# Optimization experiments

Hardware: AMD Instinct MI355X
Metric: run time of the kernel (lower is better)

## Reference

```python
import jax, jax.numpy as jnp
import numpy as np

N = 100000   # points
C = 256      # in_planes
K = 16       # nsample (idx holds 2*K neighbors)
L = 2        # num_mlplayer
NEG = 0.1    # LeakyReLU slope
EPS = 1e-5   # LayerNorm eps (torch default)

PARAM_KEYS = ['emb_w1','emb_g1','emb_b1','emb_w2','conv_w','pw_w1','pw_g1','pw_b1','pw_w2','pw_g2','pw_b2']


def layer_norm(x, g, b):
    m = x.mean(-1, keepdims=True)
    v = ((x - m) ** 2).mean(-1, keepdims=True)
    return (x - m) * jax.lax.rsqrt(v + EPS) * g + b


def calc_ppf(p, n, pg, ng):
    # standard 4-dim point-pair features: angle(n1,d), angle(n2,d), angle(n1,n2), ||d||
    d = pg - p[:, None, :]                                   # [N,2K,3]
    dist = jnp.linalg.norm(d, axis=-1, keepdims=True)
    def angle(a, b):
        cr = jnp.linalg.norm(jnp.cross(a, b), axis=-1, keepdims=True)
        dt = jnp.sum(a * b, axis=-1, keepdims=True)
        return jnp.arctan2(cr, dt)
    n1 = jnp.broadcast_to(n[:, None, :], pg.shape)
    return jnp.concatenate([angle(n1, d), angle(ng, d), angle(n1, ng), dist], -1)


def mlp_layer(p, x, idx, ppf, r, pr):
    # cart2sphere -> r-normalized radial distance, giving 4+1=5 embedding inputs
    d = p[idx] - p[:, None, :]                               # [N,K,3]
    sphere = jnp.linalg.norm(d, axis=-1, keepdims=True) / r  # [N,K,1]
    f5 = jnp.concatenate([ppf, sphere], -1)                  # [N,K,5]
    h = f5 @ pr['emb_w1']
    h = jax.nn.leaky_relu(layer_norm(h, pr['emb_g1'], pr['emb_b1']), NEG)
    pos = h @ pr['emb_w2']                                   # [N,K,C]
    g = x[idx] + pos                                         # gather + add
    # Partial_conv3 (split_cat): 1x1 conv (no bias) on first C//4 channels
    c4 = pr['conv_w'].shape[0]
    g1 = jnp.einsum('nkc,dc->nkd', g[..., :c4], pr['conv_w'])
    g = jnp.concatenate([g1, g[..., c4:]], -1)
    pooled = g.max(axis=1)                                   # max-pool over neighbors [N,C]
    h = pooled @ pr['pw_w1']
    h = jax.nn.leaky_relu(layer_norm(h, pr['pw_g1'], pr['pw_b1']), NEG)
    h = layer_norm(h @ pr['pw_w2'], pr['pw_g2'], pr['pw_b2'])
    return jax.nn.relu(h + x)                                # residual + relu


def setup_inputs():
    key = jax.random.key(0)
    ks = jax.random.split(key, 16)
    s = 0.02
    n = jax.random.normal(ks[2], (N, 3), jnp.float32)
    n = n / jnp.linalg.norm(n, axis=-1, keepdims=True)
    return {
        'p': jax.random.normal(ks[0], (N, 3), jnp.float32),
        'x': jax.random.normal(ks[1], (N, C), jnp.float32),
        'n': n,
        'idx': jax.random.randint(ks[3], (N, 2 * K), 0, N, jnp.int32),
        'r': jnp.ones((1,), jnp.float32),
        'emb_w1': jax.random.normal(ks[4], (L, 5, C), jnp.float32) * s,
        'emb_g1': jnp.ones((L, C), jnp.float32),
        'emb_b1': jnp.zeros((L, C), jnp.float32),
        'emb_w2': jax.random.normal(ks[5], (L, C, C), jnp.float32) * s,
        'conv_w': jax.random.normal(ks[6], (L, C // 4, C // 4), jnp.float32) * s,
        'pw_w1': jax.random.normal(ks[7], (L, C, 4 * C), jnp.float32) * s,
        'pw_g1': jnp.ones((L, 4 * C), jnp.float32),
        'pw_b1': jnp.zeros((L, 4 * C), jnp.float32),
        'pw_w2': jax.random.normal(ks[8], (L, 4 * C, C), jnp.float32) * s,
        'pw_g2': jnp.ones((L, C), jnp.float32),
        'pw_b2': jnp.zeros((L, C), jnp.float32),
        'proj_w': jax.random.normal(ks[9], (C, C), jnp.float32) * s,
        'proj_b': jnp.zeros((C,), jnp.float32),
    }


def reference(p, x, n, idx, r, emb_w1, emb_g1, emb_b1, emb_w2, conv_w,
              pw_w1, pw_g1, pw_b1, pw_w2, pw_g2, pw_b2, proj_w, proj_b):
    # idx is given -> group_idx = idx (queryandgroup branch skipped, as in source)
    ppf = calc_ppf(p, n, p[idx], n[idx])                     # [N,2K,4]
    idx_m, ppf_m = idx[:, :K], ppf[:, :K]                    # mlp branch uses first nsample
    stacked = [emb_w1, emb_g1, emb_b1, emb_w2, conv_w, pw_w1, pw_g1, pw_b1, pw_w2, pw_g2, pw_b2]
    h = x
    for l in range(L):
        pr = dict(zip(PARAM_KEYS, [a[l] for a in stacked]))
        h = mlp_layer(p, h, idx_m, ppf_m, r[0], pr)
    # proj_mlp; blocks=1 -> trans_block is an empty Sequential (identity)
    return h @ proj_w + proj_b
```

## Files before the change

kernel.cpp:

```cpp
#include <hip/hip_runtime.h>
#include <stdint.h>

#define N_PTS 100000
#define NPAD  100032

typedef unsigned short u16;
typedef unsigned int   u32;
using bf16x8 = __attribute__((ext_vector_type(8))) short;
using f32x4  = __attribute__((ext_vector_type(4))) float;

__device__ __forceinline__ u16 f2bf(float f) {
    u32 u = __float_as_uint(f);
    u += 0x7FFFu + ((u >> 16) & 1u);
    return (u16)(u >> 16);
}
__device__ __forceinline__ float bf2f(u16 h) {
    return __uint_as_float(((u32)h) << 16);
}

__global__ __launch_bounds__(256) void k_transpose_pad(
    const float* __restrict__ src, u16* __restrict__ dst,
    int Lc, int R, int Cc, int stride) {
    int t = blockIdx.x * 256 + threadIdx.x;
    int total = Lc * Cc * stride;
    if (t >= total) return;
    int l = t / (Cc * stride);
    int rem = t - l * (Cc * stride);
    int co = rem / stride;
    int ci = rem - co * stride;
    dst[t] = (ci < R) ? f2bf(src[((size_t)l * R + ci) * Cc + co]) : (u16)0;
}

__global__ __launch_bounds__(256) void k_cast_bf16(
    const float* __restrict__ src, u16* __restrict__ dst, int total) {
    int t = blockIdx.x * 256 + threadIdx.x;
    if (t < total) dst[t] = f2bf(src[t]);
}

__global__ __launch_bounds__(256) void k_castx8(
    const float* __restrict__ src, u16* __restrict__ dst, int total8) {
    int t = blockIdx.x * 256 + threadIdx.x;
    if (t >= total8) return;
    float4 a = *(const float4*)(src + (size_t)t * 8);
    float4 b = *(const float4*)(src + (size_t)t * 8 + 4);
    uint4 o;
    o.x = (u32)f2bf(a.x) | ((u32)f2bf(a.y) << 16);
    o.y = (u32)f2bf(a.z) | ((u32)f2bf(a.w) << 16);
    o.z = (u32)f2bf(b.x) | ((u32)f2bf(b.y) << 16);
    o.w = (u32)f2bf(b.z) | ((u32)f2bf(b.w) << 16);
    *(uint4*)(dst + (size_t)t * 8) = o;
}

__device__ __forceinline__ float angf(float ax, float ay, float az,
                                      float bx, float by, float bz) {
    float cx = ay * bz - az * by;
    float cy = az * bx - ax * bz;
    float cz = ax * by - ay * bx;
    float cr = sqrtf(cx * cx + cy * cy + cz * cz);
    float dt = ax * bx + ay * by + az * bz;
    return atan2f(cr, dt);
}

__global__ __launch_bounds__(256) void k_ppf(
    const float* __restrict__ p, const float* __restrict__ nrm,
    const int* __restrict__ idx, const float* __restrict__ r,
    u16* __restrict__ f5b) {
    int t = blockIdx.x * 256 + threadIdx.x;
    if (t >= N_PTS * 16) return;
    int i = t >> 4;
    int j = idx[(size_t)i * 32 + (t & 15)];
    float pix = p[(size_t)i*3], piy = p[(size_t)i*3+1], piz = p[(size_t)i*3+2];
    float pjx = p[(size_t)j*3], pjy = p[(size_t)j*3+1], pjz = p[(size_t)j*3+2];
    float dx = pjx - pix, dy = pjy - piy, dz = pjz - piz;
    float dist = sqrtf(dx*dx + dy*dy + dz*dz);
    float nix = nrm[(size_t)i*3], niy = nrm[(size_t)i*3+1], niz = nrm[(size_t)i*3+2];
    float njx = nrm[(size_t)j*3], njy = nrm[(size_t)j*3+1], njz = nrm[(size_t)j*3+2];
    float a1 = angf(nix, niy, niz, dx, dy, dz);
    float a2 = angf(njx, njy, njz, dx, dy, dz);
    float a3 = angf(nix, niy, niz, njx, njy, njz);
    float rinv = 1.0f / r[0];
    u16* o = f5b + (size_t)t * 5;
    o[0] = f2bf(a1); o[1] = f2bf(a2); o[2] = f2bf(a3);
    o[3] = f2bf(dist); o[4] = f2bf(dist * rinv);
}

__device__ __forceinline__ bf16x8 fixup_frag(const uint2* pk, int kt,
                                             int srcA, int srcB, bool hiT) {
    int aLx = __shfl((int)pk[2*kt].x,   srcA);
    int aHx = __shfl((int)pk[2*kt+1].x, srcA);
    int aLy = __shfl((int)pk[2*kt].y,   srcA);
    int aHy = __shfl((int)pk[2*kt+1].y, srcA);
    int bLx = __shfl((int)pk[2*kt].x,   srcB);
    int bHx = __shfl((int)pk[2*kt+1].x, srcB);
    int bLy = __shfl((int)pk[2*kt].y,   srcB);
    int bHy = __shfl((int)pk[2*kt+1].y, srcB);
    uint4 u;
    u.x = (u32)(hiT ? aHx : aLx);
    u.y = (u32)(hiT ? aHy : aLy);
    u.z = (u32)(hiT ? bHx : bLx);
    u.w = (u32)(hiT ? bHy : bLy);
    return *(bf16x8*)&u;
}

__global__ __launch_bounds__(512, 4) void k_neighbor(
    const u16*   __restrict__ xcur,
    const u16*   __restrict__ f5b,
    const int*   __restrict__ idx,
    const u16*   __restrict__ w1pad,
    const float* __restrict__ g1, const float* __restrict__ b1,
    const u16*   __restrict__ ew2tp,
    const u16*   __restrict__ convbf,
    u16*         __restrict__ pooledb)
{
    __shared__ u16 Bs[64 * 264];
    __shared__ u16 posw[8][2][16][72];
    __shared__ u16 pbounce[8][2][256];
    __shared__ int idxs[16][16];

    const int tid = threadIdx.x, w = tid >> 6, lane = tid & 63;
    const int rr = lane & 15, q = lane >> 4;
    const int i0 = blockIdx.x * 16;

    for (int o = tid * 16; o < 33792; o += 8192)
        *(uint4*)((char*)Bs + o) = *(const uint4*)((const char*)ew2tp + o);
    if (tid < 256)
        idxs[tid >> 4][tid & 15] = idx[(size_t)(i0 + (tid >> 4)) * 32 + (tid & 15)];

    const int srcA = rr + ((q & 1) << 5);
    const int srcB = srcA + 16;
    const bool hiT = (q >> 1) != 0;

    bf16x8 hfrag[2][8];
    #pragma unroll
    for (int rt = 0; rt < 2; ++rt) {
        const int pt = i0 + 2 * w + rt;
        bf16x8 a1;
        #pragma unroll
        for (int e = 0; e < 8; ++e) a1[e] = 0;
        if (q == 0) {
            const u16* fp = f5b + (size_t)(pt * 16 + rr) * 5;
            a1[0] = (short)fp[0]; a1[1] = (short)fp[1];
            a1[2] = (short)fp[2]; a1[3] = (short)fp[3];
            a1[4] = (short)fp[4];
        }
        f32x4 hacc[16];
        #pragma unroll
        for (int ct = 0; ct < 16; ++ct) {
            bf16x8 aW = *(const bf16x8*)&w1pad[(ct * 16 + rr) * 32 + q * 8];
            f32x4 z = {0.f, 0.f, 0.f, 0.f};
            hacc[ct] = __builtin_amdgcn_mfma_f32_16x16x32_bf16(aW, a1, z, 0, 0, 0);
        }
        float s = 0.f, z2 = 0.f;
        #pragma unroll
        for (int ct = 0; ct < 16; ++ct) {
            #pragma unroll
            for (int j = 0; j < 4; ++j) { float v = hacc[ct][j]; s += v; z2 += v * v; }
        }
        s  += __shfl_xor(s, 16);  s  += __shfl_xor(s, 32);
        z2 += __shfl_xor(z2, 16); z2 += __shfl_xor(z2, 32);
        float mean = s * (1.f / 256.f);
        float var = fmaxf(z2 * (1.f / 256.f) - mean * mean, 0.f);
        float rstd = 1.0f / sqrtf(var + 1e-5f);

        uint2 pk[16];
        #pragma unroll
        for (int ct = 0; ct < 16; ++ct) {
            const int c0 = ct * 16 + 4 * q;
            float4 gg = *(const float4*)&g1[c0];
            float4 bb = *(const float4*)&b1[c0];
            float v0 = (hacc[ct][0] - mean) * rstd * gg.x + bb.x;
            float v1 = (hacc[ct][1] - mean) * rstd * gg.y + bb.y;
            float v2 = (hacc[ct][2] - mean) * rstd * gg.z + bb.z;
            float v3 = (hacc[ct][3] - mean) * rstd * gg.w + bb.w;
            v0 = v0 > 0.f ? v0 : 0.1f * v0;
            v1 = v1 > 0.f ? v1 : 0.1f * v1;
            v2 = v2 > 0.f ? v2 : 0.1f * v2;
            v3 = v3 > 0.f ? v3 : 0.1f * v3;
            pk[ct].x = (u32)f2bf(v0) | ((u32)f2bf(v1) << 16);
            pk[ct].y = (u32)f2bf(v2) | ((u32)f2bf(v3) << 16);
        }
        #pragma unroll
        for (int kt = 0; kt < 8; ++kt)
            hfrag[rt][kt] = fixup_frag(pk, kt, srcA, srcB, hiT);
    }
    __syncthreads();

    const int ppt = lane >> 5, cl = lane & 31;
    const int* ixp = idxs[2 * w + ppt];

    #pragma unroll 1
    for (int p = 0; p < 4; ++p) {
        #pragma unroll
        for (int nt4 = 0; nt4 < 4; ++nt4) {
            f32x4 a0 = {0.f,0.f,0.f,0.f}, a1v = {0.f,0.f,0.f,0.f};
            #pragma unroll
            for (int kb = 0; kb < 8; ++kb) {
                bf16x8 bb = *(const bf16x8*)&Bs[(nt4 * 16 + rr) * 264 + kb * 32 + q * 8];
                a0  = __builtin_amdgcn_mfma_f32_16x16x32_bf16(hfrag[0][kb], bb, a0, 0, 0, 0);
                a1v = __builtin_amdgcn_mfma_f32_16x16x32_bf16(hfrag[1][kb], bb, a1v, 0, 0, 0);
            }
            #pragma unroll
            for (int j = 0; j < 4; ++j) {
                posw[w][0][4 * q + j][nt4 * 16 + rr] = f2bf(a0[j]);
                posw[w][1][4 * q + j][nt4 * 16 + rr] = f2bf(a1v[j]);
            }
        }
        if (p < 3) {
            __syncthreads();
            const char* src = (const char*)(ew2tp + (size_t)(p + 1) * 64 * 264);
            for (int o = tid * 16; o < 33792; o += 8192)
                *(uint4*)((char*)Bs + o) = *(const uint4*)(src + o);
        }
        if (p == 0) {
            #pragma unroll
            for (int pt = 0; pt < 2; ++pt) {
                const u16* xr = xcur + (size_t)idxs[2 * w + pt][rr] * 256;
                bf16x8 gA[2];
                #pragma unroll
                for (int kb = 0; kb < 2; ++kb) {
                    bf16x8 xa = *(const bf16x8*)(xr + kb * 32 + q * 8);
                    bf16x8 pv = *(const bf16x8*)&posw[w][pt][rr][kb * 32 + q * 8];
                    bf16x8 g;
                    #pragma unroll
                    for (int e = 0; e < 8; ++e)
                        g[e] = (short)f2bf(bf2f((u16)xa[e]) + bf2f((u16)pv[e]));
                    gA[kb] = g;
                }
                #pragma unroll
                for (int cn = 0; cn < 4; ++cn) {
                    bf16x8 cB0 = *(const bf16x8*)&convbf[(cn * 16 + rr) * 64 + q * 8];
                    bf16x8 cB1 = *(const bf16x8*)&convbf[(cn * 16 + rr) * 64 + 32 + q * 8];
                    f32x4 z = {0.f,0.f,0.f,0.f};
                    f32x4 acc = __builtin_amdgcn_mfma_f32_16x16x32_bf16(gA[0], cB0, z, 0, 0, 0);
                    acc = __builtin_amdgcn_mfma_f32_16x16x32_bf16(gA[1], cB1, acc, 0, 0, 0);
                    float m = fmaxf(fmaxf(acc[0], acc[1]), fmaxf(acc[2], acc[3]));
                    m = fmaxf(m, __shfl_xor(m, 16));
                    m = fmaxf(m, __shfl_xor(m, 32));
                    if (lane < 16) pbounce[w][pt][cn * 16 + lane] = f2bf(m);
                }
            }
        } else {
            const int cq = p * 64 + cl * 2;
            u32 xv[16];
            #pragma unroll
            for (int k = 0; k < 16; ++k)
                xv[k] = *(const u32*)(xcur + (size_t)ixp[k] * 256 + cq);
            float m0 = -3e38f, m1 = -3e38f;
            #pragma unroll
            for (int k = 0; k < 16; ++k) {
                u32 pv = *(const u32*)&posw[w][ppt][k][cl * 2];
                float gv0 = bf2f((u16)(pv & 0xffffu)) + bf2f((u16)(xv[k] & 0xffffu));
                float gv1 = bf2f((u16)(pv >> 16))     + bf2f((u16)(xv[k] >> 16));
                m0 = fmaxf(m0, gv0);
                m1 = fmaxf(m1, gv1);
            }
            *(u32*)&pbounce[w][ppt][cq] = (u32)f2bf(m0) | ((u32)f2bf(m1) << 16);
        }
        if (p < 3) __syncthreads();
    }
    {
        const int pt = lane >> 5, off = (lane & 31) * 8;
        uint4 v = *(const uint4*)&pbounce[w][pt][off];
        *(uint4*)(pooledb + (size_t)(i0 + 2 * w + pt) * 256 + off) = v;
    }
}

__global__ __launch_bounds__(512, 4) void k_pointwise(
    const u16* poolb,
    const u16* __restrict__ xresb,
    u16*       outb,
    const u16* __restrict__ b1t,
    const float* __restrict__ g1, const float* __restrict__ b1,
    const u16* __restrict__ b2t,
    const float* __restrict__ g2, const float* __restrict__ b2,
    int guardRes)
{
    __shared__ u16 hm[32 * 1032];
    __shared__ float pst[32][8][2];

    const int tid = threadIdx.x, w = tid >> 6, lane = tid & 63;
    const int rr = lane & 15, q = lane >> 4;
    const size_t R0 = (size_t)blockIdx.x * 32;

    bf16x8 afr[2][8];
    #pragma unroll
    for (int rt = 0; rt < 2; ++rt) {
        int ar = (int)R0 + rt * 16 + rr; if (ar >= N_PTS) ar = N_PTS - 1;
        const u16* arow = poolb + (size_t)ar * 256;
        #pragma unroll
        for (int kb = 0; kb < 8; ++kb)
            afr[rt][kb] = *(const bf16x8*)(arow + kb * 32 + q * 8);
    }

    #pragma unroll 2
    for (int ct = 0; ct < 8; ++ct) {
        const int co = w * 128 + ct * 16 + rr;
        const u16* bp = b1t + (size_t)co * 256 + q * 8;
        bf16x8 bb[8];
        #pragma unroll
        for (int kb = 0; kb < 8; ++kb) bb[kb] = *(const bf16x8*)(bp + kb * 32);
        f32x4 a0 = {0.f,0.f,0.f,0.f}, a1v = {0.f,0.f,0.f,0.f};
        #pragma unroll
        for (int kb = 0; kb < 8; ++kb) {
            a0  = __builtin_amdgcn_mfma_f32_16x16x32_bf16(afr[0][kb], bb[kb], a0, 0, 0, 0);
            a1v = __builtin_amdgcn_mfma_f32_16x16x32_bf16(afr[1][kb], bb[kb], a1v, 0, 0, 0);
        }
        #pragma unroll
        for (int j = 0; j < 4; ++j) {
            hm[(4 * q + j) * 1032 + co]      = f2bf(a0[j]);
            hm[(16 + 4 * q + j) * 1032 + co] = f2bf(a1v[j]);
        }
    }
    __syncthreads();

    {
        const int row = tid >> 4;
        const int t16 = tid & 15;
        u32* hm32 = (u32*)hm;
        const int base = row * 516;
        float s = 0.f, z = 0.f;
        #pragma unroll 8
        for (int e = 0; e < 32; ++e) {
            u32 pk = hm32[base + t16 + 16 * e];
            float v0 = bf2f((u16)(pk & 0xffffu)), v1 = bf2f((u16)(pk >> 16));
            s += v0 + v1; z += v0 * v0 + v1 * v1;
        }
        s += __shfl_xor(s, 1); s += __shfl_xor(s, 2);
        s += __shfl_xor(s, 4); s += __shfl_xor(s, 8);
        z += __shfl_xor(z, 1); z += __shfl_xor(z, 2);
        z += __shfl_xor(z, 4); z += __shfl_xor(z, 8);
        float mean = s * (1.f / 1024.f);
        float var = fmaxf(z * (1.f / 1024.f) - mean * mean, 0.f);
        float rstd = 1.0f / sqrtf(var + 1e-5f);
        #pragma unroll 4
        for (int e = 0; e < 32; ++e) {
            const int cidx = t16 + 16 * e;
            u32 pk = hm32[base + cidx];
            const int c = cidx * 2;
            float2 gg = *(const float2*)&g1[c];
            float2 bbv = *(const float2*)&b1[c];
            float v0 = (bf2f((u16)(pk & 0xffffu)) - mean) * rstd * gg.x + bbv.x;
            float v1 = (bf2f((u16)(pk >> 16))     - mean) * rstd * gg.y + bbv.y;
            v0 = v0 > 0.f ? v0 : 0.1f * v0;
            v1 = v1 > 0.f ? v1 : 0.1f * v1;
            hm32[base + cidx] = (u32)f2bf(v0) | ((u32)f2bf(v1) << 16);
        }
    }
    __syncthreads();

    f32x4 acc2[2][2];
    #pragma unroll
    for (int ct = 0; ct < 2; ++ct) {
        const int cB = w * 32 + ct * 16 + rr;
        const u16* bp = b2t + (size_t)cB * 1024 + q * 8;
        f32x4 c0 = {0.f,0.f,0.f,0.f}, c1 = {0.f,0.f,0.f,0.f};
        #pragma unroll 8
        for (int kb = 0; kb < 32; ++kb) {
            bf16x8 b  = *(const bf16x8*)(bp + kb * 32);
            bf16x8 a0 = *(const bf16x8*)&hm[rr * 1032 + kb * 32 + q * 8];
            bf16x8 a1 = *(const bf16x8*)&hm[(16 + rr) * 1032 + kb * 32 + q * 8];
            c0 = __builtin_amdgcn_mfma_f32_16x16x32_bf16(a0, b, c0, 0, 0, 0);
            c1 = __builtin_amdgcn_mfma_f32_16x16x32_bf16(a1, b, c1, 0, 0, 0);
        }
        acc2[0][ct] = c0; acc2[1][ct] = c1;
    }

    #pragma unroll
    for (int rt = 0; rt < 2; ++rt) {
        #pragma unroll
        for (int j = 0; j < 4; ++j) {
            float s = acc2[rt][0][j] + acc2[rt][1][j];
            float z = acc2[rt][0][j] * acc2[rt][0][j] + acc2[rt][1][j] * acc2[rt][1][j];
            s += __shfl_xor(s, 1); s += __shfl_xor(s, 2);
            s += __shfl_xor(s, 4); s += __shfl_xor(s, 8);
            z += __shfl_xor(z, 1); z += __shfl_xor(z, 2);
            z += __shfl_xor(z, 4); z += __shfl_xor(z, 8);
            if (rr == 0) {
                pst[rt * 16 + 4 * q + j][w][0] = s;
                pst[rt * 16 + 4 * q + j][w][1] = z;
            }
        }
    }
    __syncthreads();

    #pragma unroll
    for (int rt = 0; rt < 2; ++rt) {
        float mean2[4], rstd2[4];
        #pragma unroll
        for (int j = 0; j < 4; ++j) {
            const int row = rt * 16 + 4 * q + j;
            float s = 0.f, z = 0.f;
            #pragma unroll
            for (int k = 0; k < 8; ++k) { s += pst[row][k][0]; z += pst[row][k][1]; }
            float mean = s * (1.f / 256.f);
            float var = fmaxf(z * (1.f / 256.f) - mean * mean, 0.f);
            mean2[j] = mean;
            rstd2[j] = 1.0f / sqrtf(var + 1e-5f);
        }
        #pragma unroll
        for (int ct = 0; ct < 2; ++ct) {
            const int c = w * 32 + ct * 16 + rr;
            const float gg = g2[c], bb = b2[c];
            #pragma unroll
            for (int j = 0; j < 4; ++j) {
                const size_t row = R0 + rt * 16 + 4 * q + j;
                float v = (acc2[rt][ct][j] - mean2[j]) * rstd2[j] * gg + bb;
                float xv = 0.f;
                if (!guardRes || row < (size_t)N_PTS) xv = bf2f(xresb[row * 256 + c]);
                float o = v + xv;
                outb[row * 256 + c] = f2bf(o > 0.f ? o : 0.f);
            }
        }
    }
}

__global__ __launch_bounds__(512, 4) void k_proj(
    const u16*   __restrict__ xinb,
    const u16*   __restrict__ pjtp,
    const float* __restrict__ pb,
    float*       __restrict__ out)
{
    __shared__ u16 Bs[128 * 264];
    const int tid = threadIdx.x, w = tid >> 6, lane = tid & 63;
    const int rr = lane & 15, q = lane >> 4;
    const size_t R0 = (size_t)blockIdx.x * 128 + (size_t)w * 16;

    int arn = (int)R0 + rr; if (arn >= N_PTS) arn = N_PTS - 1;
    const u16* arow = xinb + (size_t)arn * 256;
    bf16x8 afr[8];
    #pragma unroll
    for (int kb = 0; kb < 8; ++kb)
        afr[kb] = *(const bf16x8*)(arow + kb * 32 + q * 8);

    #pragma unroll 1
    for (int h = 0; h < 2; ++h) {
        if (h) __syncthreads();
        for (int o = tid * 16; o < 67584; o += 8192)
            *(uint4*)((char*)Bs + o) = *(const uint4*)((const char*)(pjtp + h * 128 * 264) + o);
        __syncthreads();
        #pragma unroll 2
        for (int nt8 = 0; nt8 < 8; ++nt8) {
            f32x4 acc = {0.f, 0.f, 0.f, 0.f};
            #pragma unroll
            for (int kb = 0; kb < 8; ++kb) {
                bf16x8 b = *(const bf16x8*)&Bs[(nt8 * 16 + rr) * 264 + kb * 32 + q * 8];
                acc = __builtin_amdgcn_mfma_f32_16x16x32_bf16(afr[kb], b, acc, 0, 0, 0);
            }
            const int c = h * 128 + nt8 * 16 + rr;
            const float bias = pb[c];
            #pragma unroll
            for (int j = 0; j < 4; ++j) {
                const size_t row = R0 + 4 * q + j;
                if (row < (size_t)N_PTS) out[row * 256 + c] = acc[j] + bias;
            }
        }
    }
}

extern "C" void kernel_launch(void* const* d_in, const int* in_sizes, int n_in,
                              void* d_out, int out_size, void* d_ws, size_t ws_size,
                              hipStream_t stream) {
    const float* p      = (const float*)d_in[0];
    const float* x      = (const float*)d_in[1];
    const float* nn     = (const float*)d_in[2];
    const int*   idx    = (const int*)d_in[3];
    const float* r      = (const float*)d_in[4];
    const float* emb_w1 = (const float*)d_in[5];
    const float* emb_g1 = (const float*)d_in[6];
    const float* emb_b1 = (const float*)d_in[7];
    const float* emb_w2 = (const float*)d_in[8];
    const float* conv_w = (const float*)d_in[9];
    const float* pw_w1  = (const float*)d_in[10];
    const float* pw_g1  = (const float*)d_in[11];
    const float* pw_b1  = (const float*)d_in[12];
    const float* pw_w2  = (const float*)d_in[13];
    const float* pw_g2  = (const float*)d_in[14];
    const float* pw_b2  = (const float*)d_in[15];
    const float* proj_w = (const float*)d_in[16];
    const float* proj_b = (const float*)d_in[17];
    float* out = (float*)d_out;

    char* ws = (char*)d_ws;
    const size_t SZB = (size_t)NPAD * 256 * sizeof(u16);
    u16* xb0 = (u16*)ws;
    u16* PB  = (u16*)(ws + SZB);
    u16* h1B = (u16*)(ws + 2 * SZB);
    u16* f5b = (u16*)(ws + 3 * SZB);
    u16* wb  = f5b + (size_t)N_PTS * 16 * 5;
    u16* ew2tp  = wb;
    u16* pjtp   = ew2tp + 2 * 256 * 264;
    u16* w1pad  = pjtp + 256 * 264;
    u16* convbf = w1pad + 2 * 256 * 32;
    u16* b1t    = convbf + 2 * 64 * 64;
    u16* b2t    = b1t + 2 * 1024 * 256;

    k_transpose_pad<<<(2*256*264 + 255)/256, 256, 0, stream>>>(emb_w2, ew2tp, 2, 256, 256, 264);
    k_transpose_pad<<<(256*264 + 255)/256, 256, 0, stream>>>(proj_w, pjtp, 1, 256, 256, 264);
    k_transpose_pad<<<(2*256*32 + 255)/256, 256, 0, stream>>>(emb_w1, w1pad, 2, 5, 256, 32);
    k_transpose_pad<<<(2*1024*256 + 255)/256, 256, 0, stream>>>(pw_w1, b1t, 2, 256, 1024, 256);
    k_transpose_pad<<<(2*256*1024 + 255)/256, 256, 0, stream>>>(pw_w2, b2t, 2, 1024, 256, 1024);
    k_cast_bf16<<<(2*64*64 + 255)/256, 256, 0, stream>>>(conv_w, convbf, 2*64*64);

    k_castx8<<<(N_PTS*256/8 + 255)/256, 256, 0, stream>>>(x, xb0, N_PTS*256/8);
    k_ppf<<<(N_PTS * 16 + 255)/256, 256, 0, stream>>>(p, nn, idx, r, f5b);

    k_neighbor<<<N_PTS/16, 512, 0, stream>>>(xb0, f5b, idx, w1pad, emb_g1, emb_b1,
                                             ew2tp, convbf, PB);
    k_pointwise<<<NPAD/32, 512, 0, stream>>>(PB, xb0, h1B, b1t, pw_g1, pw_b1,
                                             b2t, pw_g2, pw_b2, 1);
    k_neighbor<<<N_PTS/16, 512, 0, stream>>>(h1B, f5b, idx, w1pad + 256*32,
                                             emb_g1 + 256, emb_b1 + 256,
                                             ew2tp + 256*264, convbf + 64*64, xb0);
    k_pointwise<<<NPAD/32, 512, 0, stream>>>(xb0, h1B, PB, b1t + 1024*256,
                                             pw_g1 + 1024, pw_b1 + 1024,
                                             b2t + 256*1024, pw_g2 + 256, pw_b2 + 256, 0);
    k_proj<<<(NPAD + 127)/128, 512, 0, stream>>>(PB, pjtp, proj_b, out);
}
```

Measured before the change: 2.262 ms.

## Software-pipeline neighbor feature gathers ahead of per-quarter position GEMMs

Unrolls the four-quarter loop of the gather/pool kernel and issues the global gathers of neighbor features for the next channel quarter before the current quarter's MFMA GEMM and pooling. The first-quarter x loads are also hoisted before the embedding MLP, and an extra barrier is added so idxs is visible early. The aim is to hide gather latency behind compute. The cost is higher register pressure from the double-buffered xv arrays, which may lower occupancy or cause spills.

```diff
diff --git a/kernel.cpp b/kernel.cpp
--- a/kernel.cpp
+++ b/kernel.cpp
@@ -125,10 +125,21 @@
         *(uint4*)((char*)Bs + o) = *(const uint4*)((const char*)ew2tp + o);
     if (tid < 256)
         idxs[tid >> 4][tid & 15] = idx[(size_t)(i0 + (tid >> 4)) * 32 + (tid & 15)];
+    __syncthreads();
 
     const int srcA = rr + ((q & 1) << 5);
     const int srcB = srcA + 16;
     const bool hiT = (q >> 1) != 0;
+    const int ppt = lane >> 5, cl = lane & 31;
+    const int* ixp = idxs[2 * w + ppt];
+
+    bf16x8 xcv[2][2];
+    #pragma unroll
+    for (int pt = 0; pt < 2; ++pt) {
+        const u16* xr = xcur + (size_t)idxs[2 * w + pt][rr] * 256;
+        xcv[pt][0] = *(const bf16x8*)(xr + q * 8);
+        xcv[pt][1] = *(const bf16x8*)(xr + 32 + q * 8);
+    }
 
     bf16x8 hfrag[2][8];
     #pragma unroll
@@ -183,13 +194,8 @@
         for (int kt = 0; kt < 8; ++kt)
             hfrag[rt][kt] = fixup_frag(pk, kt, srcA, srcB, hiT);
     }
-    __syncthreads();
-
-    const int ppt = lane >> 5, cl = lane & 31;
-    const int* ixp = idxs[2 * w + ppt];
-
-    #pragma unroll 1
-    for (int p = 0; p < 4; ++p) {
+
+    auto do_gemm = [&]() {
         #pragma unroll
         for (int nt4 = 0; nt4 < 4; ++nt4) {
             f32x4 a0 = {0.f,0.f,0.f,0.f}, a1v = {0.f,0.f,0.f,0.f};
@@ -205,59 +211,81 @@
                 posw[w][1][4 * q + j][nt4 * 16 + rr] = f2bf(a1v[j]);
             }
         }
-        if (p < 3) {
-            __syncthreads();
-            const char* src = (const char*)(ew2tp + (size_t)(p + 1) * 64 * 264);
-            for (int o = tid * 16; o < 33792; o += 8192)
-                *(uint4*)((char*)Bs + o) = *(const uint4*)(src + o);
-        }
-        if (p == 0) {
-            #pragma unroll
-            for (int pt = 0; pt < 2; ++pt) {
-                const u16* xr = xcur + (size_t)idxs[2 * w + pt][rr] * 256;
-                bf16x8 gA[2];
-                #pragma unroll
-                for (int kb = 0; kb < 2; ++kb) {
-                    bf16x8 xa = *(const bf16x8*)(xr + kb * 32 + q * 8);
-                    bf16x8 pv = *(const bf16x8*)&posw[w][pt][rr][kb * 32 + q * 8];
-                    bf16x8 g;
-                    #pragma unroll
-                    for (int e = 0; e < 8; ++e)
-                        g[e] = (short)f2bf(bf2f((u16)xa[e]) + bf2f((u16)pv[e]));
-                    gA[kb] = g;
-                }
-                #pragma unroll
-                for (int cn = 0; cn < 4; ++cn) {
-                    bf16x8 cB0 = *(const bf16x8*)&convbf[(cn * 16 + rr) * 64 + q * 8];
-                    bf16x8 cB1 = *(const bf16x8*)&convbf[(cn * 16 + rr) * 64 + 32 + q * 8];
-                    f32x4 z = {0.f,0.f,0.f,0.f};
-                    f32x4 acc = __builtin_amdgcn_mfma_f32_16x16x32_bf16(gA[0], cB0, z, 0, 0, 0);
-                    acc = __builtin_amdgcn_mfma_f32_16x16x32_bf16(gA[1], cB1, acc, 0, 0, 0);
-                    float m = fmaxf(fmaxf(acc[0], acc[1]), fmaxf(acc[2], acc[3]));
-                    m = fmaxf(m, __shfl_xor(m, 16));
-                    m = fmaxf(m, __shfl_xor(m, 32));
-                    if (lane < 16) pbounce[w][pt][cn * 16 + lane] = f2bf(m);
-                }
-            }
-        } else {
-            const int cq = p * 64 + cl * 2;
-            u32 xv[16];
-            #pragma unroll
-            for (int k = 0; k < 16; ++k)
-                xv[k] = *(const u32*)(xcur + (size_t)ixp[k] * 256 + cq);
-            float m0 = -3e38f, m1 = -3e38f;
-            #pragma unroll
-            for (int k = 0; k < 16; ++k) {
-                u32 pv = *(const u32*)&posw[w][ppt][k][cl * 2];
-                float gv0 = bf2f((u16)(pv & 0xffffu)) + bf2f((u16)(xv[k] & 0xffffu));
-                float gv1 = bf2f((u16)(pv >> 16))     + bf2f((u16)(xv[k] >> 16));
-                m0 = fmaxf(m0, gv0);
-                m1 = fmaxf(m1, gv1);
-            }
-            *(u32*)&pbounce[w][ppt][cq] = (u32)f2bf(m0) | ((u32)f2bf(m1) << 16);
-        }
-        if (p < 3) __syncthreads();
-    }
+    };
+    auto stage_q = [&](int pnext) {
+        const char* src = (const char*)(ew2tp + (size_t)pnext * 64 * 264);
+        for (int o = tid * 16; o < 33792; o += 8192)
+            *(uint4*)((char*)Bs + o) = *(const uint4*)(src + o);
+    };
+    auto load_q = [&](int p, u32 (&xv)[16]) {
+        const int cq = p * 64 + cl * 2;
+        #pragma unroll
+        for (int k = 0; k < 16; ++k)
+            xv[k] = *(const u32*)(xcur + (size_t)ixp[k] * 256 + cq);
+    };
+    auto pool_q = [&](int p, const u32 (&xv)[16]) {
+        const int cq = p * 64 + cl * 2;
+        float m0 = -3e38f, m1 = -3e38f;
+        #pragma unroll
+        for (int k = 0; k < 16; ++k) {
+            u32 pv = *(const u32*)&posw[w][ppt][k][cl * 2];
+            m0 = fmaxf(m0, bf2f((u16)(pv & 0xffffu)) + bf2f((u16)(xv[k] & 0xffffu)));
+            m1 = fmaxf(m1, bf2f((u16)(pv >> 16))     + bf2f((u16)(xv[k] >> 16)));
+        }
+        *(u32*)&pbounce[w][ppt][cq] = (u32)f2bf(m0) | ((u32)f2bf(m1) << 16);
+    };
+
+    u32 xvA[16], xvB[16];
+    load_q(1, xvA);
+
+    do_gemm();
+    __syncthreads();
+    stage_q(1);
+    #pragma unroll
+    for (int pt = 0; pt < 2; ++pt) {
+        bf16x8 gA[2];
+        #pragma unroll
+        for (int kb = 0; kb < 2; ++kb) {
+            bf16x8 xa = xcv[pt][kb];
+            bf16x8 pv = *(const bf16x8*)&posw[w][pt][rr][kb * 32 + q * 8];
+            bf16x8 g;
+            #pragma unroll
+            for (int e = 0; e < 8; ++e)
+                g[e] = (short)f2bf(bf2f((u16)xa[e]) + bf2f((u16)pv[e]));
+            gA[kb] = g;
+        }
+        #pragma unroll
+        for (int cn = 0; cn < 4; ++cn) {
+            bf16x8 cB0 = *(const bf16x8*)&convbf[(cn * 16 + rr) * 64 + q * 8];
+            bf16x8 cB1 = *(const bf16x8*)&convbf[(cn * 16 + rr) * 64 + 32 + q * 8];
+            f32x4 z = {0.f,0.f,0.f,0.f};
+            f32x4 acc = __builtin_amdgcn_mfma_f32_16x16x32_bf16(gA[0], cB0, z, 0, 0, 0);
+            acc = __builtin_amdgcn_mfma_f32_16x16x32_bf16(gA[1], cB1, acc, 0, 0, 0);
+            float m = fmaxf(fmaxf(acc[0], acc[1]), fmaxf(acc[2], acc[3]));
+            m = fmaxf(m, __shfl_xor(m, 16));
+            m = fmaxf(m, __shfl_xor(m, 32));
+            if (lane < 16) pbounce[w][pt][cn * 16 + lane] = f2bf(m);
+        }
+    }
+    load_q(2, xvB);
+    __syncthreads();
+
+    do_gemm();
+    __syncthreads();
+    stage_q(2);
+    pool_q(1, xvA);
+    load_q(3, xvA);
+    __syncthreads();
+
+    do_gemm();
+    __syncthreads();
+    stage_q(3);
+    pool_q(2, xvB);
+    __syncthreads();
+
+    do_gemm();
+    pool_q(3, xvA);
+
     {
         const int pt = lane >> 5, off = (lane & 31) * 8;
         uint4 v = *(const uint4*)&pbounce[w][pt][off];
```

Result: slower. 2.367 ms (+4.6%).
